# Performance work log

Hardware: AMD Instinct MI355X
Metric: run time of the kernel (lower is better)

The kernel has to match this reference:

```python
import jax, jax.numpy as jnp
import numpy as np

BITS = 4
MAXQ = 15          # (1 << BITS) - 1
PACK = 32 // BITS  # 8 values packed per int32


def dequantize(qweight, qzeros, scales, g_idx):
    """GPTQ 4-bit dequant. qweight: [K//8, N] int32, qzeros: [G, N//8] int32,
    scales: [G, N] float, g_idx: [K] int32 -> dense W [K, N] float."""
    N = qweight.shape[1]
    shifts = (jnp.arange(PACK, dtype=jnp.uint32) * BITS)  # [8]
    qw = qweight.astype(jnp.uint32)
    # unpack along K: k = row*8 + j  (matches shifter = (k % 8) * bits)
    w_int = ((qw[:, None, :] >> shifts[None, :, None]) & MAXQ).reshape(-1, N)  # [K, N]
    qz = qzeros.astype(jnp.uint32)
    # unpack along N: n = col*8 + j  (matches zeros_shifter = (n % 8) * bits)
    z_int = ((qz[:, :, None] >> shifts[None, None, :]) & MAXQ).reshape(qzeros.shape[0], -1) + 1  # [G, N]
    dt = scales.dtype
    # group-wise dequant: w = (q - zero) * scale, gathered per-row via g_idx
    return (w_int.astype(dt) - z_int[g_idx].astype(dt)) * scales[g_idx]


def setup_inputs() -> dict:
    key = jax.random.key(0)
    k1, k2, k3, k4, k5 = jax.random.split(key, 5)
    M, K, N, GS = 128, 4096, 11008, 128
    G = K // GS
    x = jax.random.normal(k1, (M, K), dtype=jnp.float32)
    qweight = jax.random.randint(k2, (K // PACK, N), 0, 2147483647, dtype=jnp.int32)
    qzeros = jax.random.randint(k3, (G, N // PACK), 0, 2147483647, dtype=jnp.int32)
    scales = jax.random.uniform(k4, (G, N), dtype=jnp.float32, minval=0.001, maxval=0.01)
    bias = jax.random.normal(k5, (N,), dtype=jnp.float32)
    g_idx = (jnp.arange(K, dtype=jnp.int32) // GS).astype(jnp.int32)
    return {"x": x, "qweight": qweight, "qzeros": qzeros, "scales": scales,
            "bias": bias, "g_idx": g_idx}


def reference(x, qweight, qzeros, scales, bias, g_idx):
    w = dequantize(qweight, qzeros, scales, g_idx)  # [K, N]
    return x @ w + bias
```

## Files before the change

### kernel.cpp

```cpp
#include <hip/hip_runtime.h>
#include <stdint.h>


#define M_DIM 128
#define K_DIM 4096
#define N_DIM 11008
#define GS    128
#define NG    32
#define SPLIT 4
#define GPB   (NG / SPLIT)
#define NB    (N_DIM / 64)
#define PART_ELEMS ((size_t)NB * 4 * 2048)

typedef _Float16 half8  __attribute__((ext_vector_type(8)));
typedef _Float16 half2t __attribute__((ext_vector_type(2)));
typedef _Float16 half4t __attribute__((ext_vector_type(4)));
typedef float    f32x4  __attribute__((ext_vector_type(4)));

__global__ void k_prep(const float* __restrict__ x, const int* __restrict__ qzeros,
                       const float* __restrict__ scales,
                       _Float16* __restrict__ xh, _Float16* __restrict__ szp) {
    int b = blockIdx.x, tid = threadIdx.x;
    if (b < 512) {
        int i = (b * 256 + tid) * 4;
        float4 v = *(const float4*)(x + i);
        half4t o;
        o[0] = (_Float16)v.x; o[1] = (_Float16)v.y;
        o[2] = (_Float16)v.z; o[3] = (_Float16)v.w;
        *(half4t*)(xh + i) = o;
    } else {
        b -= 512;
        int g = b / 43;
        int n = (b - g * 43) * 256 + tid;
        unsigned qz = (unsigned)qzeros[g * (N_DIM / 8) + (n >> 3)];
        float s  = scales[g * N_DIM + n];
        float z1 = (float)((qz >> ((n & 7) * 4)) & 15u) + 1.0f;
        half2t o;
        o[0] = (_Float16)s;
        o[1] = (_Float16)(-(z1 * s));
        *(half2t*)(szp + (size_t)(g * N_DIM + n) * 2) = o;
    }
}

__device__ __forceinline__ void load_lds16(const void* g, void* l) {
    __builtin_amdgcn_global_load_lds(
        (const __attribute__((address_space(1))) unsigned int*)g,
        (__attribute__((address_space(3))) unsigned int*)l, 16, 0, 0);
}

__device__ __forceinline__ half8 dequant8(unsigned q, half2t S2, half2t Z2) {
    const half2t BIAS = __builtin_bit_cast(half2t, 0x64006400u);
    half2t w[4];
#pragma unroll
    for (int p = 0; p < 4; ++p) {
        unsigned r = __builtin_amdgcn_perm(q, q, 0x00010001u * (unsigned)p);
        unsigned t = (r & 0x00F0000Fu) | 0x64006400u;
        w[p] = __builtin_elementwise_fma(__builtin_bit_cast(half2t, t) - BIAS, S2, Z2);
    }
    half4t lo = __builtin_shufflevector(w[0], w[1], 0, 1, 2, 3);
    half4t hi = __builtin_shufflevector(w[2], w[3], 0, 1, 2, 3);
    return __builtin_shufflevector(lo, hi, 0, 1, 2, 3, 4, 5, 6, 7);
}

__global__ __launch_bounds__(512, 4)
void k_gemm(const _Float16* __restrict__ xh,
            const int*      __restrict__ qweight,
            const _Float16* __restrict__ szp,
            _Float16*       __restrict__ part)
{
    __shared__ _Float16 As[2][128 * 128];

    const int tid  = threadIdx.x;
    const int lane = tid & 63;
    const int w    = tid >> 6;
    const int ns   = w & 3;
    const int kh   = w >> 2;
    const int q    = lane >> 4;
    const int lr   = lane & 15;

    const int n0 = blockIdx.x * 64;
    const int g0 = blockIdx.y * GPB;
    const int ncol = n0 + ns * 16 + lr;

    f32x4 acc[8];
#pragma unroll
    for (int f = 0; f < 8; ++f)
        acc[f] = (f32x4){0.f, 0.f, 0.f, 0.f};

    int cm[4], ckb[4];
#pragma unroll
    for (int it = 0; it < 4; ++it) {
        int c = it * 512 + tid;
        cm[it]  = c >> 4;
        ckb[it] = (c & 15) ^ (cm[it] & 15);
    }
    const int wave_lds = w * 64 * 8;

#pragma unroll
    for (int it = 0; it < 4; ++it)
        load_lds16(xh + (size_t)cm[it] * K_DIM + g0 * GS + ckb[it] * 8,
                   &As[0][it * 512 * 8 + wave_lds]);
    unsigned qwn[2];
    half2t   szn;
#pragma unroll
    for (int t = 0; t < 2; ++t)
        qwn[t] = (unsigned)qweight[(size_t)(g0 * 16 + (kh * 2 + t) * 4 + q) * N_DIM + ncol];
    szn = *(const half2t*)(szp + ((size_t)g0 * N_DIM + ncol) * 2);

    int p = 0;
    for (int g = 0; g < GPB; ++g) {
        unsigned qw[2];
        half2t   sz;
#pragma unroll
        for (int i = 0; i < 2; ++i) qw[i] = qwn[i];
        sz = szn;

        __syncthreads();

        if (g + 1 < GPB) {
            int gn = g0 + g + 1;
#pragma unroll
            for (int it = 0; it < 4; ++it)
                load_lds16(xh + (size_t)cm[it] * K_DIM + gn * GS + ckb[it] * 8,
                           &As[p ^ 1][it * 512 * 8 + wave_lds]);
#pragma unroll
            for (int t = 0; t < 2; ++t)
                qwn[t] = (unsigned)qweight[(size_t)(gn * 16 + (kh * 2 + t) * 4 + q) * N_DIM + ncol];
            szn = *(const half2t*)(szp + ((size_t)gn * N_DIM + ncol) * 2);
        }

        half2t S2, Z2;
        S2[0] = sz[0];
        S2[1] = sz[0] * (_Float16)0.0625f;
        Z2[0] = sz[1];
        Z2[1] = sz[1];

#pragma unroll
        for (int t = 0; t < 2; ++t) {
            const int kk = kh * 2 + t;
            half8 bf = dequant8(qw[t], S2, Z2);
            const int kb2 = (kk * 4 + q) ^ lr;
#pragma unroll
            for (int f = 0; f < 8; ++f) {
                int m = f * 16 + lr;
                half8 af = *(const half8*)(&As[p][m * 128 + kb2 * 8]);
                acc[f] = __builtin_amdgcn_mfma_f32_16x16x32_f16(af, bf, acc[f], 0, 0, 0);
            }
        }
        p ^= 1;
    }

    __syncthreads();
    float* red = (float*)&As[0][0];
    if (kh == 1) {
#pragma unroll
        for (int f = 0; f < 8; ++f)
            *(f32x4*)(red + ns * 2048 + f * 256 + lane * 4) = acc[f];
    }
    __syncthreads();
    if (kh == 0) {
        _Float16* ph = part + (size_t)blockIdx.y * PART_ELEMS
                     + (size_t)(blockIdx.x * 4 + ns) * 2048;
#pragma unroll
        for (int f = 0; f < 8; ++f) {
            f32x4 o = acc[f] + *(const f32x4*)(red + ns * 2048 + f * 256 + lane * 4);
            half4t ov;
#pragma unroll
            for (int r = 0; r < 4; ++r) ov[r] = (_Float16)o[r];
            *(half4t*)(ph + (f * 64 + lane) * 4) = ov;
        }
    }
}

__global__ void k_reduce(const _Float16* __restrict__ part, const float* __restrict__ bias,
                         float* __restrict__ out) {
    int t = blockIdx.x * 256 + threadIdx.x;
    int lane = t & 63, f = (t >> 6) & 7, ns = (t >> 9) & 3, nb = t >> 11;
    int q = lane >> 4, lr = lane & 15;
    int m0 = f * 16 + q * 4;
    int n  = nb * 64 + ns * 16 + lr;
    f32x4 sv = (f32x4){0.f, 0.f, 0.f, 0.f};
#pragma unroll
    for (int s = 0; s < SPLIT; ++s) {
        half4t v = *(const half4t*)(part + s * PART_ELEMS + (size_t)t * 4);
#pragma unroll
        for (int r = 0; r < 4; ++r) sv[r] += (float)v[r];
    }
    float b = bias[n];
#pragma unroll
    for (int r = 0; r < 4; ++r)
        out[(size_t)(m0 + r) * N_DIM + n] = sv[r] + b;
}

extern "C" void kernel_launch(void* const* d_in, const int* in_sizes, int n_in,
                              void* d_out, int out_size, void* d_ws, size_t ws_size,
                              hipStream_t stream) {
    const float* x       = (const float*)d_in[0];
    const int*   qweight = (const int*)d_in[1];
    const int*   qzeros  = (const int*)d_in[2];
    const float* scales  = (const float*)d_in[3];
    const float* bias    = (const float*)d_in[4];

    char* ws = (char*)d_ws;
    _Float16* xh   = (_Float16*)ws;
    _Float16* szp  = (_Float16*)(ws + 1048576);
    _Float16* part = (_Float16*)(ws + 1048576 + 1409024);

    k_prep  <<<dim3(1888),         dim3(256), 0, stream>>>(x, qzeros, scales, xh, szp);
    k_gemm  <<<dim3(NB, SPLIT),    dim3(512), 0, stream>>>(xh, qweight, szp, part);
    k_reduce<<<dim3(1376),         dim3(256), 0, stream>>>(part, bias, (float*)d_out);
}
```

Baseline: 101.0 us.

## Fuse split-K reduction into GEMM via last-block atomic counter

Result: slower. 231.7 us (+129.5%).

```diff
diff --git a/kernel.cpp b/kernel.cpp
--- a/kernel.cpp
+++ b/kernel.cpp
@@ -19,7 +19,8 @@
 
 __global__ void k_prep(const float* __restrict__ x, const int* __restrict__ qzeros,
                        const float* __restrict__ scales,
-                       _Float16* __restrict__ xh, _Float16* __restrict__ szp) {
+                       _Float16* __restrict__ xh, _Float16* __restrict__ szp,
+                       int* __restrict__ cnt) {
     int b = blockIdx.x, tid = threadIdx.x;
     if (b < 512) {
         int i = (b * 256 + tid) * 4;
@@ -28,7 +29,7 @@
         o[0] = (_Float16)v.x; o[1] = (_Float16)v.y;
         o[2] = (_Float16)v.z; o[3] = (_Float16)v.w;
         *(half4t*)(xh + i) = o;
-    } else {
+    } else if (b < 1888) {
         b -= 512;
         int g = b / 43;
         int n = (b - g * 43) * 256 + tid;
@@ -39,6 +40,8 @@
         o[0] = (_Float16)s;
         o[1] = (_Float16)(-(z1 * s));
         *(half2t*)(szp + (size_t)(g * N_DIM + n) * 2) = o;
+    } else {
+        if (tid < NB) cnt[tid] = 0;
     }
 }
 
@@ -66,9 +69,13 @@
 void k_gemm(const _Float16* __restrict__ xh,
             const int*      __restrict__ qweight,
             const _Float16* __restrict__ szp,
-            _Float16*       __restrict__ part)
+            _Float16*       __restrict__ part,
+            const float*    __restrict__ bias,
+            float*          __restrict__ out,
+            int*            __restrict__ cnt)
 {
     __shared__ _Float16 As[2][128 * 128];
+    __shared__ int lastflag;
 
     const int tid  = threadIdx.x;
     const int lane = tid & 63;
@@ -158,38 +165,47 @@
             *(f32x4*)(red + ns * 2048 + f * 256 + lane * 4) = acc[f];
     }
     __syncthreads();
+
     if (kh == 0) {
+#pragma unroll
+        for (int f = 0; f < 8; ++f)
+            acc[f] += *(const f32x4*)(red + ns * 2048 + f * 256 + lane * 4);
         _Float16* ph = part + (size_t)blockIdx.y * PART_ELEMS
                      + (size_t)(blockIdx.x * 4 + ns) * 2048;
 #pragma unroll
         for (int f = 0; f < 8; ++f) {
-            f32x4 o = acc[f] + *(const f32x4*)(red + ns * 2048 + f * 256 + lane * 4);
             half4t ov;
 #pragma unroll
-            for (int r = 0; r < 4; ++r) ov[r] = (_Float16)o[r];
+            for (int r = 0; r < 4; ++r) ov[r] = (_Float16)acc[f][r];
             *(half4t*)(ph + (f * 64 + lane) * 4) = ov;
         }
     }
-}
-
-__global__ void k_reduce(const _Float16* __restrict__ part, const float* __restrict__ bias,
-                         float* __restrict__ out) {
-    int t = blockIdx.x * 256 + threadIdx.x;
-    int lane = t & 63, f = (t >> 6) & 7, ns = (t >> 9) & 3, nb = t >> 11;
-    int q = lane >> 4, lr = lane & 15;
-    int m0 = f * 16 + q * 4;
-    int n  = nb * 64 + ns * 16 + lr;
-    f32x4 sv = (f32x4){0.f, 0.f, 0.f, 0.f};
-#pragma unroll
-    for (int s = 0; s < SPLIT; ++s) {
-        half4t v = *(const half4t*)(part + s * PART_ELEMS + (size_t)t * 4);
-#pragma unroll
-        for (int r = 0; r < 4; ++r) sv[r] += (float)v[r];
-    }
-    float b = bias[n];
-#pragma unroll
-    for (int r = 0; r < 4; ++r)
-        out[(size_t)(m0 + r) * N_DIM + n] = sv[r] + b;
+    __threadfence();
+    __syncthreads();
+    if (tid == 0)
+        lastflag = (atomicAdd(&cnt[blockIdx.x], 1) == SPLIT - 1) ? 1 : 0;
+    __syncthreads();
+
+    if (lastflag && kh == 0) {
+        __threadfence();
+        float bv = bias[ncol];
+        const int my = blockIdx.y;
+#pragma unroll
+        for (int f = 0; f < 8; ++f) {
+            f32x4 o = acc[f];
+#pragma unroll
+            for (int sp = 0; sp < SPLIT; ++sp) {
+                if (sp == my) continue;
+                half4t v = *(const half4t*)(part + (size_t)sp * PART_ELEMS
+                          + (size_t)(blockIdx.x * 4 + ns) * 2048 + (f * 64 + lane) * 4);
+#pragma unroll
+                for (int r = 0; r < 4; ++r) o[r] += (float)v[r];
+            }
+#pragma unroll
+            for (int r = 0; r < 4; ++r)
+                out[(size_t)(f * 16 + q * 4 + r) * N_DIM + ncol] = o[r] + bv;
+        }
+    }
 }
 
 extern "C" void kernel_launch(void* const* d_in, const int* in_sizes, int n_in,
@@ -204,9 +220,10 @@
     char* ws = (char*)d_ws;
     _Float16* xh   = (_Float16*)ws;
     _Float16* szp  = (_Float16*)(ws + 1048576);
-    _Float16* part = (_Float16*)(ws + 1048576 + 1409024);
-
-    k_prep  <<<dim3(1888),         dim3(256), 0, stream>>>(x, qzeros, scales, xh, szp);
-    k_gemm  <<<dim3(NB, SPLIT),    dim3(512), 0, stream>>>(xh, qweight, szp, part);
-    k_reduce<<<dim3(1376),         dim3(256), 0, stream>>>(part, bias, (float*)d_out);
-}
+    _Float16* part = (_Float16*)(ws + 2457600);
+    int*      cnt  = (int*)(ws + 2457600 + 4 * 2818048);
+
+    k_prep<<<dim3(1889),        dim3(256), 0, stream>>>(x, qzeros, scales, xh, szp, cnt);
+    k_gemm<<<dim3(NB, SPLIT),   dim3(512), 0, stream>>>(xh, qweight, szp, part,
+                                                        bias, (float*)d_out, cnt);
+}
```

## Remove split-K and fuse bias epilogue into GEMM, dropping reduce kernel

Applied to the files above, without the earlier changes.

Measured after the change: 103.1 us. 2.1% more time.

```diff
diff --git a/kernel.cpp b/kernel.cpp
--- a/kernel.cpp
+++ b/kernel.cpp
@@ -7,10 +7,8 @@
 #define N_DIM 11008
 #define GS    128
 #define NG    32
-#define SPLIT 4
-#define GPB   (NG / SPLIT)
+#define GPB   NG
 #define NB    (N_DIM / 64)
-#define PART_ELEMS ((size_t)NB * 4 * 2048)
 
 typedef _Float16 half8  __attribute__((ext_vector_type(8)));
 typedef _Float16 half2t __attribute__((ext_vector_type(2)));
@@ -66,7 +64,8 @@
 void k_gemm(const _Float16* __restrict__ xh,
             const int*      __restrict__ qweight,
             const _Float16* __restrict__ szp,
-            _Float16*       __restrict__ part)
+            const float*    __restrict__ bias,
+            float*          __restrict__ out)
 {
     __shared__ _Float16 As[2][128 * 128];
 
@@ -79,7 +78,6 @@
     const int lr   = lane & 15;
 
     const int n0 = blockIdx.x * 64;
-    const int g0 = blockIdx.y * GPB;
     const int ncol = n0 + ns * 16 + lr;
 
     f32x4 acc[8];
@@ -98,14 +96,14 @@
 
 #pragma unroll
     for (int it = 0; it < 4; ++it)
-        load_lds16(xh + (size_t)cm[it] * K_DIM + g0 * GS + ckb[it] * 8,
+        load_lds16(xh + (size_t)cm[it] * K_DIM + ckb[it] * 8,
                    &As[0][it * 512 * 8 + wave_lds]);
     unsigned qwn[2];
     half2t   szn;
 #pragma unroll
     for (int t = 0; t < 2; ++t)
-        qwn[t] = (unsigned)qweight[(size_t)(g0 * 16 + (kh * 2 + t) * 4 + q) * N_DIM + ncol];
-    szn = *(const half2t*)(szp + ((size_t)g0 * N_DIM + ncol) * 2);
+        qwn[t] = (unsigned)qweight[(size_t)((kh * 2 + t) * 4 + q) * N_DIM + ncol];
+    szn = *(const half2t*)(szp + (size_t)ncol * 2);
 
     int p = 0;
     for (int g = 0; g < GPB; ++g) {
@@ -118,7 +116,7 @@
         __syncthreads();
 
         if (g + 1 < GPB) {
-            int gn = g0 + g + 1;
+            int gn = g + 1;
 #pragma unroll
             for (int it = 0; it < 4; ++it)
                 load_lds16(xh + (size_t)cm[it] * K_DIM + gn * GS + ckb[it] * 8,
@@ -159,37 +157,15 @@
     }
     __syncthreads();
     if (kh == 0) {
-        _Float16* ph = part + (size_t)blockIdx.y * PART_ELEMS
-                     + (size_t)(blockIdx.x * 4 + ns) * 2048;
+        float bv = bias[ncol];
 #pragma unroll
         for (int f = 0; f < 8; ++f) {
             f32x4 o = acc[f] + *(const f32x4*)(red + ns * 2048 + f * 256 + lane * 4);
-            half4t ov;
 #pragma unroll
-            for (int r = 0; r < 4; ++r) ov[r] = (_Float16)o[r];
-            *(half4t*)(ph + (f * 64 + lane) * 4) = ov;
+            for (int r = 0; r < 4; ++r)
+                out[(size_t)(f * 16 + q * 4 + r) * N_DIM + ncol] = o[r] + bv;
         }
     }
-}
-
-__global__ void k_reduce(const _Float16* __restrict__ part, const float* __restrict__ bias,
-                         float* __restrict__ out) {
-    int t = blockIdx.x * 256 + threadIdx.x;
-    int lane = t & 63, f = (t >> 6) & 7, ns = (t >> 9) & 3, nb = t >> 11;
-    int q = lane >> 4, lr = lane & 15;
-    int m0 = f * 16 + q * 4;
-    int n  = nb * 64 + ns * 16 + lr;
-    f32x4 sv = (f32x4){0.f, 0.f, 0.f, 0.f};
-#pragma unroll
-    for (int s = 0; s < SPLIT; ++s) {
-        half4t v = *(const half4t*)(part + s * PART_ELEMS + (size_t)t * 4);
-#pragma unroll
-        for (int r = 0; r < 4; ++r) sv[r] += (float)v[r];
-    }
-    float b = bias[n];
-#pragma unroll
-    for (int r = 0; r < 4; ++r)
-        out[(size_t)(m0 + r) * N_DIM + n] = sv[r] + b;
 }
 
 extern "C" void kernel_launch(void* const* d_in, const int* in_sizes, int n_in,
@@ -202,11 +178,9 @@
     const float* bias    = (const float*)d_in[4];
 
     char* ws = (char*)d_ws;
-    _Float16* xh   = (_Float16*)ws;
-    _Float16* szp  = (_Float16*)(ws + 1048576);
-    _Float16* part = (_Float16*)(ws + 1048576 + 1409024);
+    _Float16* xh  = (_Float16*)ws;
+    _Float16* szp = (_Float16*)(ws + 1048576);
 
-    k_prep  <<<dim3(1888),         dim3(256), 0, stream>>>(x, qzeros, scales, xh, szp);
-    k_gemm  <<<dim3(NB, SPLIT),    dim3(512), 0, stream>>>(xh, qweight, szp, part);
-    k_reduce<<<dim3(1376),         dim3(256), 0, stream>>>(part, bias, (float*)d_out);
+    k_prep<<<dim3(1888), dim3(256), 0, stream>>>(x, qzeros, scales, xh, szp);
+    k_gemm<<<dim3(NB),   dim3(512), 0, stream>>>(xh, qweight, szp, bias, (float*)d_out);
 }
```

## Switch GEMM to 32x32x16 MFMA with four-way K split across waves

Applied to the files above, without the earlier changes.

Measured after the change: 101.7 us. No clear change (+0.8%).

```diff
diff --git a/kernel.cpp b/kernel.cpp
--- a/kernel.cpp
+++ b/kernel.cpp
@@ -10,12 +10,13 @@
 #define SPLIT 4
 #define GPB   (NG / SPLIT)
 #define NB    (N_DIM / 64)
-#define PART_ELEMS ((size_t)NB * 4 * 2048)
+#define PART_ELEMS ((size_t)NB * 2 * 4096)
 
 typedef _Float16 half8  __attribute__((ext_vector_type(8)));
 typedef _Float16 half2t __attribute__((ext_vector_type(2)));
 typedef _Float16 half4t __attribute__((ext_vector_type(4)));
 typedef float    f32x4  __attribute__((ext_vector_type(4)));
+typedef float    f32x16 __attribute__((ext_vector_type(16)));
 
 __global__ void k_prep(const float* __restrict__ x, const int* __restrict__ qzeros,
                        const float* __restrict__ scales,
@@ -73,19 +74,21 @@
     const int tid  = threadIdx.x;
     const int lane = tid & 63;
     const int w    = tid >> 6;
-    const int ns   = w & 3;
-    const int kh   = w >> 2;
-    const int q    = lane >> 4;
-    const int lr   = lane & 15;
+    const int nsl  = w & 1;
+    const int kq   = w >> 1;
+    const int hl   = lane >> 5;
+    const int l31  = lane & 31;
 
     const int n0 = blockIdx.x * 64;
     const int g0 = blockIdx.y * GPB;
-    const int ncol = n0 + ns * 16 + lr;
-
-    f32x4 acc[8];
-#pragma unroll
-    for (int f = 0; f < 8; ++f)
-        acc[f] = (f32x4){0.f, 0.f, 0.f, 0.f};
+    const int ncol = n0 + nsl * 32 + l31;
+
+    f32x16 acc[4];
+#pragma unroll
+    for (int f = 0; f < 4; ++f)
+#pragma unroll
+        for (int e = 0; e < 16; ++e)
+            acc[f][e] = 0.f;
 
     int cm[4], ckb[4];
 #pragma unroll
@@ -103,8 +106,8 @@
     unsigned qwn[2];
     half2t   szn;
 #pragma unroll
-    for (int t = 0; t < 2; ++t)
-        qwn[t] = (unsigned)qweight[(size_t)(g0 * 16 + (kh * 2 + t) * 4 + q) * N_DIM + ncol];
+    for (int mf = 0; mf < 2; ++mf)
+        qwn[mf] = (unsigned)qweight[(size_t)(g0 * 16 + kq * 4 + mf * 2 + hl) * N_DIM + ncol];
     szn = *(const half2t*)(szp + ((size_t)g0 * N_DIM + ncol) * 2);
 
     int p = 0;
@@ -124,8 +127,8 @@
                 load_lds16(xh + (size_t)cm[it] * K_DIM + gn * GS + ckb[it] * 8,
                            &As[p ^ 1][it * 512 * 8 + wave_lds]);
 #pragma unroll
-            for (int t = 0; t < 2; ++t)
-                qwn[t] = (unsigned)qweight[(size_t)(gn * 16 + (kh * 2 + t) * 4 + q) * N_DIM + ncol];
+            for (int mf = 0; mf < 2; ++mf)
+                qwn[mf] = (unsigned)qweight[(size_t)(gn * 16 + kq * 4 + mf * 2 + hl) * N_DIM + ncol];
             szn = *(const half2t*)(szp + ((size_t)gn * N_DIM + ncol) * 2);
         }
 
@@ -136,15 +139,14 @@
         Z2[1] = sz[1];
 
 #pragma unroll
-        for (int t = 0; t < 2; ++t) {
-            const int kk = kh * 2 + t;
-            half8 bf = dequant8(qw[t], S2, Z2);
-            const int kb2 = (kk * 4 + q) ^ lr;
-#pragma unroll
-            for (int f = 0; f < 8; ++f) {
-                int m = f * 16 + lr;
-                half8 af = *(const half8*)(&As[p][m * 128 + kb2 * 8]);
-                acc[f] = __builtin_amdgcn_mfma_f32_16x16x32_f16(af, bf, acc[f], 0, 0, 0);
+        for (int mf = 0; mf < 2; ++mf) {
+            half8 bf = dequant8(qw[mf], S2, Z2);
+            const int kb_sw = (kq * 4 + mf * 2 + hl) ^ (lane & 15);
+#pragma unroll
+            for (int f = 0; f < 4; ++f) {
+                int m = f * 32 + l31;
+                half8 af = *(const half8*)(&As[p][m * 128 + kb_sw * 8]);
+                acc[f] = __builtin_amdgcn_mfma_f32_32x32x16_f16(af, bf, acc[f], 0, 0, 0);
             }
         }
         p ^= 1;
@@ -152,33 +154,68 @@
 
     __syncthreads();
     float* red = (float*)&As[0][0];
-    if (kh == 1) {
-#pragma unroll
-        for (int f = 0; f < 8; ++f)
-            *(f32x4*)(red + ns * 2048 + f * 256 + lane * 4) = acc[f];
-    }
-    __syncthreads();
-    if (kh == 0) {
+    if (kq >= 2) {
+        float* rw = red + ((nsl << 1) | (kq - 2)) * 4096;
+#pragma unroll
+        for (int f = 0; f < 4; ++f)
+#pragma unroll
+            for (int rg = 0; rg < 4; ++rg) {
+                f32x4 v = { acc[f][rg*4+0], acc[f][rg*4+1],
+                            acc[f][rg*4+2], acc[f][rg*4+3] };
+                *(f32x4*)(rw + (f * 4 + rg) * 256 + lane * 4) = v;
+            }
+    }
+    __syncthreads();
+    if (kq < 2) {
+        const float* rd = red + ((nsl << 1) | kq) * 4096;
+#pragma unroll
+        for (int f = 0; f < 4; ++f)
+#pragma unroll
+            for (int rg = 0; rg < 4; ++rg) {
+                f32x4 v = *(const f32x4*)(rd + (f * 4 + rg) * 256 + lane * 4);
+#pragma unroll
+                for (int r = 0; r < 4; ++r) acc[f][rg*4+r] += v[r];
+            }
+    }
+    __syncthreads();
+    if (kq == 1) {
+        float* rw = red + nsl * 4096;
+#pragma unroll
+        for (int f = 0; f < 4; ++f)
+#pragma unroll
+            for (int rg = 0; rg < 4; ++rg) {
+                f32x4 v = { acc[f][rg*4+0], acc[f][rg*4+1],
+                            acc[f][rg*4+2], acc[f][rg*4+3] };
+                *(f32x4*)(rw + (f * 4 + rg) * 256 + lane * 4) = v;
+            }
+    }
+    __syncthreads();
+    if (kq == 0) {
+        const float* rd = red + nsl * 4096;
         _Float16* ph = part + (size_t)blockIdx.y * PART_ELEMS
-                     + (size_t)(blockIdx.x * 4 + ns) * 2048;
-#pragma unroll
-        for (int f = 0; f < 8; ++f) {
-            f32x4 o = acc[f] + *(const f32x4*)(red + ns * 2048 + f * 256 + lane * 4);
-            half4t ov;
-#pragma unroll
-            for (int r = 0; r < 4; ++r) ov[r] = (_Float16)o[r];
-            *(half4t*)(ph + (f * 64 + lane) * 4) = ov;
-        }
+                     + (size_t)(blockIdx.x * 2 + nsl) * 4096;
+#pragma unroll
+        for (int f = 0; f < 4; ++f)
+#pragma unroll
+            for (int rg = 0; rg < 4; ++rg) {
+                f32x4 v = *(const f32x4*)(rd + (f * 4 + rg) * 256 + lane * 4);
+                half4t ov;
+#pragma unroll
+                for (int r = 0; r < 4; ++r)
+                    ov[r] = (_Float16)(acc[f][rg*4+r] + v[r]);
+                *(half4t*)(ph + ((f * 4 + rg) * 64 + lane) * 4) = ov;
+            }
     }
 }
 
 __global__ void k_reduce(const _Float16* __restrict__ part, const float* __restrict__ bias,
                          float* __restrict__ out) {
     int t = blockIdx.x * 256 + threadIdx.x;
-    int lane = t & 63, f = (t >> 6) & 7, ns = (t >> 9) & 3, nb = t >> 11;
-    int q = lane >> 4, lr = lane & 15;
-    int m0 = f * 16 + q * 4;
-    int n  = nb * 64 + ns * 16 + lr;
+    int lane = t & 63, fr = (t >> 6) & 15, nslot = t >> 10;
+    int f = fr >> 2, rg = fr & 3;
+    int nb = nslot >> 1, nsl = nslot & 1;
+    int row0 = f * 32 + rg * 8 + ((lane >> 5) << 2);
+    int col  = nb * 64 + nsl * 32 + (lane & 31);
     f32x4 sv = (f32x4){0.f, 0.f, 0.f, 0.f};
 #pragma unroll
     for (int s = 0; s < SPLIT; ++s) {
@@ -186,10 +223,10 @@
 #pragma unroll
         for (int r = 0; r < 4; ++r) sv[r] += (float)v[r];
     }
-    float b = bias[n];
+    float b = bias[col];
 #pragma unroll
     for (int r = 0; r < 4; ++r)
-        out[(size_t)(m0 + r) * N_DIM + n] = sv[r] + b;
+        out[(size_t)(row0 + r) * N_DIM + col] = sv[r] + b;
 }
 
 extern "C" void kernel_launch(void* const* d_in, const int* in_sizes, int n_in,
```
